# Performance work log

Measured on AMD Instinct MI355X. Metric: run time of the kernel, lower is better.

The kernel has to match this reference:

```python
import jax, jax.numpy as jnp
import numpy as np

T = 0.07        # temperature (hardcoded in CCM)
BN_EPS = 1e-5   # torch BatchNorm1d default eps (eval mode, running stats)


def _l2norm(x):
    # torch F.normalize(dim=1): x / max(||x||, 1e-12)
    n = jnp.linalg.norm(x, axis=1, keepdims=True)
    return x / jnp.maximum(n, 1e-12)


def _attn(q, k):
    # cosine similarity scaled by 1/t and 1/sqrt(num_keys)
    scale = jnp.asarray(k.shape[0], q.dtype) ** 0.5
    return (_l2norm(q) @ _l2norm(k).T) / T / scale


def setup_inputs() -> dict:
    key = jax.random.key(0)
    ks = jax.random.split(key, 24)
    D, N, BS, C, H = 2048, 1024, 64, 65, 128
    f32 = jnp.float32
    def g(k, shape, scale=1.0):
        return jax.random.normal(k, shape, f32) * scale
    return {
        "all_f": g(ks[0], (BS, D)),
        "embedding": _l2norm(g(ks[1], (N, D))),  # memory queue (normalized at init)
        "all_y": jax.random.randint(ks[2], (BS,), 0, C),
        "head_w1": g(ks[3], (D, H), 1.0 / np.sqrt(D)),
        "head_b1": jnp.zeros((H,), f32),
        "head_g": jax.random.uniform(ks[4], (H,), f32) + 0.5,
        "head_beta": g(ks[5], (H,), 0.1),
        "head_rm": g(ks[6], (H,), 0.1),
        "head_rv": jax.random.uniform(ks[7], (H,), f32) + 0.5,
        "head_w2": g(ks[8], (H, H), 1.0 / np.sqrt(H)),
        "head_b2": jnp.zeros((H,), f32),
        "mix_w1": g(ks[9], (2 * H, H), 1.0 / np.sqrt(2 * H)),
        "mix_b1": jnp.zeros((H,), f32),
        "mix_g": jax.random.uniform(ks[10], (H,), f32) + 0.5,
        "mix_beta": g(ks[11], (H,), 0.1),
        "mix_rm": g(ks[12], (H,), 0.1),
        "mix_rv": jax.random.uniform(ks[13], (H,), f32) + 0.5,
        "mix_w2": g(ks[14], (H, D), 1.0 / np.sqrt(H)),
        "mix_b2": jnp.zeros((D,), f32),
        "clf_w": g(ks[15], (D, C), 1.0 / np.sqrt(D)),
        "clf_b": jnp.zeros((C,), f32),
    }


def reference(all_f, embedding, all_y,
              head_w1, head_b1, head_g, head_beta, head_rm, head_rv, head_w2, head_b2,
              mix_w1, mix_b1, mix_g, mix_beta, mix_rm, mix_rv, mix_w2, mix_b2,
              clf_w, clf_b):
    # CCM.causal(all_f, embedding, all_y): returns [bs, num_classes]
    H = head_b2.shape[0]
    # z|x attention over the memory queue
    z_x = jax.nn.softmax(_attn(all_f, embedding), axis=-1)          # [bs, N]

    def head(x):
        h = x @ head_w1 + head_b1
        h = (h - head_rm) * jax.lax.rsqrt(head_rv + BN_EPS) * head_g + head_beta
        return jax.nn.relu(h) @ head_w2 + head_b2                   # [., 128]

    hf = head(all_f)        # [bs, 128]
    hz = head(embedding)    # [N, 128]
    # mixer layer 1 on concat([hf, hz]) decomposed into two matmuls + broadcast add
    h1 = hf @ mix_w1[:H] + mix_b1                                   # [bs, 128]
    h1 = h1[:, None, :] + (hz @ mix_w1[H:])[None, :, :]             # [bs, N, 128]
    h1 = (h1 - mix_rm) * jax.lax.rsqrt(mix_rv + BN_EPS) * mix_g + mix_beta
    h1 = jax.nn.relu(h1)
    mixed = h1 @ mix_w2 + mix_b2                                    # [bs, N, D]
    y_zx = jax.nn.softmax(mixed @ clf_w + clf_b, axis=-1)           # [bs, N, C] = p(y|z,x)
    # p(x): self-attention row-sums, softmax over the batch (all_y given -> this branch)
    p_x = jax.nn.softmax(_attn(all_f, all_f).sum(axis=1), axis=0)   # [bs]
    sum_x = jnp.einsum('b,bnc->nc', p_x, y_zx)                      # [N, C]
    return z_x @ sum_x                                              # [bs, C]
```

## Files before the change

### kernel.cpp

```cpp
#include <hip/hip_runtime.h>
#include <hip/hip_bf16.h>
#include <math.h>

#define D   2048
#define NQ  1024
#define BSZ 64
#define NC  65
#define HD  128

#define OFF_SCALEH 0
#define OFF_CH     128
#define OFF_BZC    256
#define OFF_BAC    384
#define OFF_BVEC   512
#define OFF_PXP    640
#define OFF_WC     896
#define OFF_A2T    6016
#define OFF_B2     14208
#define OFF_SP     145280
#define OFF_SUMX   669568
#define OFF_FNB    751488
#define OFF_AFB    817024
#define OFF_EMBB   882560
#define OFF_W1T    1931136
#define OFF_WZT    2062208
#define OFF_WAT    2070400
#define OFF_MW2B   2078592
#define OFF_CWT    2226048

typedef __attribute__((ext_vector_type(8))) short    bf16x8;
typedef __attribute__((ext_vector_type(4))) float    f32x4;
typedef __attribute__((ext_vector_type(8))) unsigned short u16x8;
typedef __attribute__((ext_vector_type(2))) unsigned short u16x2;

__device__ inline unsigned short f2b(float v) {
    __hip_bfloat16 h = __float2bfloat16(v);
    return __builtin_bit_cast(unsigned short, h);
}

__global__ void __launch_bounds__(256) k_prep(const float* __restrict__ all_f,
                                              const float* __restrict__ emb,
                                              const float* __restrict__ head_w1,
                                              const float* __restrict__ head_b1,
                                              const float* __restrict__ head_g,
                                              const float* __restrict__ head_beta,
                                              const float* __restrict__ head_rm,
                                              const float* __restrict__ head_rv,
                                              const float* __restrict__ head_w2,
                                              const float* __restrict__ head_b2,
                                              const float* __restrict__ mix_w1,
                                              const float* __restrict__ mix_b1,
                                              const float* __restrict__ mix_g,
                                              const float* __restrict__ mix_beta,
                                              const float* __restrict__ mix_rm,
                                              const float* __restrict__ mix_rv,
                                              const float* __restrict__ mix_w2,
                                              const float* __restrict__ mix_b2,
                                              const float* __restrict__ clf_w,
                                              float* __restrict__ ws) {
    __shared__ float sbuf[128*66];
    int bid = blockIdx.x, t = threadIdx.x;
    if (bid == 0) {
        int h = t & 127, jq = t >> 7;
        float sb = 0.f, sa = 0.f;
        #pragma unroll 8
        for (int j = jq*64; j < jq*64 + 64; ++j) {
            float b2v = head_b2[j];
            sb = fmaf(b2v, mix_w1[(HD + j)*HD + h], sb);
            sa = fmaf(b2v, mix_w1[j*HD + h], sa);
        }
        sbuf[jq*256 + h]       = sb;
        sbuf[jq*256 + 128 + h] = sa;
        __syncthreads();
        if (jq == 0) {
            float s = head_g[h] * rsqrtf(head_rv[h] + 1e-5f);
            ws[OFF_SCALEH + h] = s;
            ws[OFF_CH + h] = (head_b1[h] - head_rm[h]) * s + head_beta[h];
            float ms = mix_g[h] * rsqrtf(mix_rv[h] + 1e-5f);
            float msh = mix_beta[h] - mix_rm[h] * ms;
            float sbT = sbuf[h] + sbuf[256 + h];
            float saT = sbuf[128 + h] + sbuf[256 + 128 + h];
            ws[OFF_BZC + h] = sbT * ms;
            ws[OFF_BAC + h] = fmaf(saT + mix_b1[h], ms, msh);
        }
    } else if (bid < 129) {
        int j = bid - 1;
        int h = t & 127, which = t >> 7;
        const float* M1 = mix_w1 + (which ? 0 : HD*HD);
        float ms = mix_g[h] * rsqrtf(mix_rv[h] + 1e-5f);
        float acc = 0.f;
        #pragma unroll 8
        for (int k = 0; k < HD; ++k)
            acc = fmaf(head_w2[j*HD + k], M1[k*HD + h], acc);
        unsigned short* dst = (unsigned short*)(ws + (which ? OFF_WAT : OFF_WZT));
        dst[h*HD + j] = f2b(acc * ms);
    } else if (bid < 147) {
        int r0 = (bid - 129) * 8;
        unsigned short* dst = (unsigned short*)(ws + OFF_MW2B);
        int i0 = t * 8;
        for (int rr = 0; rr < 8; ++rr) {
            int r = r0 + rr;
            u16x8 o;
            if (r < HD || r == HD) {
                const float* src = (r < HD) ? (mix_w2 + (size_t)r * D) : mix_b2;
                float4 f1 = *(const float4*)(src + i0);
                float4 f2 = *(const float4*)(src + i0 + 4);
                o[0]=f2b(f1.x); o[1]=f2b(f1.y); o[2]=f2b(f1.z); o[3]=f2b(f1.w);
                o[4]=f2b(f2.x); o[5]=f2b(f2.y); o[6]=f2b(f2.z); o[7]=f2b(f2.w);
            } else {
                o[0]=0;o[1]=0;o[2]=0;o[3]=0;o[4]=0;o[5]=0;o[6]=0;o[7]=0;
            }
            *(u16x8*)(dst + (size_t)r*D + i0) = o;
        }
    } else if (bid < 163) {
        int k0 = (bid - 147) * 128;
        float (*tile)[66] = (float(*)[66])sbuf;
        for (int i = t; i < 128*65; i += 256) {
            int r = i / 65;
            tile[r][i - 65*r] = clf_w[(size_t)k0*65 + i];
        }
        __syncthreads();
        unsigned short* cwt = (unsigned short*)(ws + OFF_CWT);
        for (int idx = t; idx < 80*16; idx += 256) {
            int c = idx >> 4, kq = idx & 15;
            u16x8 v;
            #pragma unroll
            for (int j = 0; j < 8; ++j)
                v[j] = (c < NC) ? f2b(tile[kq*8 + j][c]) : (unsigned short)0;
            *(u16x8*)(cwt + (size_t)c*D + k0 + kq*8) = v;
        }
    } else if (bid < 227) {
        int b = bid - 163;
        const float* src = all_f + (size_t)b * D;
        int i0 = t * 8;
        float4 f1 = *(const float4*)(src + i0);
        float4 f2 = *(const float4*)(src + i0 + 4);
        float s = f1.x*f1.x + f1.y*f1.y + f1.z*f1.z + f1.w*f1.w
                + f2.x*f2.x + f2.y*f2.y + f2.z*f2.z + f2.w*f2.w;
        sbuf[t] = s; __syncthreads();
        for (int k = 128; k > 0; k >>= 1) { if (t < k) sbuf[t] += sbuf[t + k]; __syncthreads(); }
        float rn = 1.f / fmaxf(sqrtf(sbuf[0]), 1e-12f);
        unsigned short* fnb = (unsigned short*)(ws + OFF_FNB) + (size_t)b * D;
        unsigned short* afb = (unsigned short*)(ws + OFF_AFB) + (size_t)b * D;
        u16x8 on, oa;
        on[0]=f2b(f1.x*rn); on[1]=f2b(f1.y*rn); on[2]=f2b(f1.z*rn); on[3]=f2b(f1.w*rn);
        on[4]=f2b(f2.x*rn); on[5]=f2b(f2.y*rn); on[6]=f2b(f2.z*rn); on[7]=f2b(f2.w*rn);
        oa[0]=f2b(f1.x); oa[1]=f2b(f1.y); oa[2]=f2b(f1.z); oa[3]=f2b(f1.w);
        oa[4]=f2b(f2.x); oa[5]=f2b(f2.y); oa[6]=f2b(f2.z); oa[7]=f2b(f2.w);
        *(u16x8*)(fnb + i0) = on;
        *(u16x8*)(afb + i0) = oa;
    } else if (bid < 483) {
        int n0 = (bid - 227) * 4;
        unsigned short* dst = (unsigned short*)(ws + OFF_EMBB);
        int i0 = t * 8;
        for (int r = 0; r < 4; ++r) {
            const float* src = emb + (size_t)(n0 + r) * D;
            float4 f1 = *(const float4*)(src + i0);
            float4 f2 = *(const float4*)(src + i0 + 4);
            u16x8 o;
            o[0]=f2b(f1.x); o[1]=f2b(f1.y); o[2]=f2b(f1.z); o[3]=f2b(f1.w);
            o[4]=f2b(f2.x); o[5]=f2b(f2.y); o[6]=f2b(f2.z); o[7]=f2b(f2.w);
            *(u16x8*)(dst + (size_t)(n0 + r)*D + i0) = o;
        }
    } else {
        int rb = bid - 483;
        float (*tile)[33] = (float(*)[33])sbuf;
        int k0 = (rb >> 2) * 128, h0 = (rb & 3) * 32;
        int hh = t & 31, kk = t >> 5;
        for (int r = 0; r < 16; ++r)
            tile[kk + r*8][hh] = head_w1[(size_t)(k0 + kk + r*8)*HD + h0 + hh];
        __syncthreads();
        unsigned short* dst = (unsigned short*)(ws + OFF_W1T);
        int kcol = (t & 63) * 2, hrow = t >> 6;
        for (int r = 0; r < 8; ++r) {
            int h = hrow + r*4;
            u16x2 v;
            v[0] = f2b(tile[kcol][h]);
            v[1] = f2b(tile[kcol + 1][h]);
            *(u16x2*)(dst + (size_t)(h0 + h)*D + k0 + kcol) = v;
        }
    }
}

__global__ void __launch_bounds__(512) k_main(const float* __restrict__ clf_b,
                                              float* __restrict__ ws) {
    __shared__ float part[2][32][128];
    __shared__ unsigned short ush[32][136];
    __shared__ float wcp[8][16][16];
    int bid = blockIdx.x, t = threadIdx.x;
    int lane = t & 63, wv = t >> 6;
    int row16 = lane & 15, kgrp = lane >> 4;
    if (bid < 128) {
        const unsigned short* fnb  = (const unsigned short*)(ws + OFF_FNB);
        const unsigned short* embb = (const unsigned short*)(ws + OFF_EMBB);
        int nt = bid & 15, ks = bid >> 4;
        int b0 = (wv & 3) * 16;
        int n0 = nt*64 + (wv >> 2) * 32;
        const unsigned short* Ap = fnb  + (size_t)(b0 + row16)*D + ks*256 + kgrp*8;
        const unsigned short* B0 = embb + (size_t)(n0 + row16)*D + ks*256 + kgrp*8;
        const unsigned short* B1 = B0 + 16*D;
        f32x4 a0 = {0,0,0,0}, a1 = {0,0,0,0};
        #pragma unroll
        for (int s = 0; s < 8; ++s) {
            bf16x8 a = *(const bf16x8*)(Ap + s*32);
            a0 = __builtin_amdgcn_mfma_f32_16x16x32_bf16(a, *(const bf16x8*)(B0 + s*32), a0, 0, 0, 0);
            a1 = __builtin_amdgcn_mfma_f32_16x16x32_bf16(a, *(const bf16x8*)(B1 + s*32), a1, 0, 0, 0);
        }
        float* Sp = ws + OFF_SP + (size_t)ks * BSZ * NQ;
        #pragma unroll
        for (int r = 0; r < 4; ++r) {
            float* rowp = Sp + (size_t)(b0 + kgrp*4 + r)*NQ + n0;
            rowp[row16]      = a0[r];
            rowp[16 + row16] = a1[r];
        }
    } else if (bid < 162) {
        int tile = bid - 128;
        bool isF = tile >= 32;
        const unsigned short* Arow = isF
            ? (const unsigned short*)(ws + OFF_AFB) + (size_t)(tile - 32) * 32 * D
            : (const unsigned short*)(ws + OFF_EMBB) + (size_t)tile * 32 * D;
        const unsigned short* w1t = (const unsigned short*)(ws + OFF_W1T);
        int hgrp = wv & 3, kh = wv >> 2;
        const unsigned short* Ap = Arow + (size_t)row16*D + kh*1024 + kgrp*8;
        const unsigned short* B0 = w1t + (size_t)(hgrp*32 + row16)*D + kh*1024 + kgrp*8;
        const unsigned short* B1 = B0 + 16*D;
        f32x4 h00 = {0,0,0,0}, h01 = {0,0,0,0}, h10 = {0,0,0,0}, h11 = {0,0,0,0};
        #pragma unroll 4
        for (int s = 0; s < 32; ++s) {
            bf16x8 a0 = *(const bf16x8*)(Ap + s*32);
            bf16x8 a1 = *(const bf16x8*)(Ap + 16*D + s*32);
            bf16x8 b0 = *(const bf16x8*)(B0 + s*32);
            bf16x8 b1 = *(const bf16x8*)(B1 + s*32);
            h00 = __builtin_amdgcn_mfma_f32_16x16x32_bf16(a0, b0, h00, 0, 0, 0);
            h01 = __builtin_amdgcn_mfma_f32_16x16x32_bf16(a0, b1, h01, 0, 0, 0);
            h10 = __builtin_amdgcn_mfma_f32_16x16x32_bf16(a1, b0, h10, 0, 0, 0);
            h11 = __builtin_amdgcn_mfma_f32_16x16x32_bf16(a1, b1, h11, 0, 0, 0);
        }
        int mb = kgrp*4, hc0 = hgrp*32 + row16, hc1 = hc0 + 16;
        #pragma unroll
        for (int r = 0; r < 4; ++r) {
            part[kh][mb + r][hc0]      = h00[r];
            part[kh][mb + r][hc1]      = h01[r];
            part[kh][16 + mb + r][hc0] = h10[r];
            part[kh][16 + mb + r][hc1] = h11[r];
        }
        __syncthreads();
        {
            int row = t >> 4, cg = (t & 15) * 8;
            #pragma unroll
            for (int j = 0; j < 8; ++j) {
                int col = cg + j;
                float v = part[0][row][col] + part[1][row][col];
                ush[row][col] = f2b(fmaxf(fmaf(v, ws[OFF_SCALEH + col], ws[OFF_CH + col]), 0.f));
            }
        }
        __syncthreads();
        {
            int rt = wv >> 2, wv2 = wv & 3;
            const unsigned short* wt = (const unsigned short*)(ws + (isF ? OFF_WAT : OFF_WZT));
            const unsigned short* W0 = wt + (size_t)(wv2*32 + row16)*HD + kgrp*8;
            const unsigned short* W1b = W0 + 16*HD;
            f32x4 o0 = {0,0,0,0}, o1 = {0,0,0,0};
            #pragma unroll
            for (int s = 0; s < 4; ++s) {
                bf16x8 a = *(const bf16x8*)(&ush[rt*16 + row16][s*32 + kgrp*8]);
                o0 = __builtin_amdgcn_mfma_f32_16x16x32_bf16(a, *(const bf16x8*)(W0 + s*32), o0, 0, 0, 0);
                o1 = __builtin_amdgcn_mfma_f32_16x16x32_bf16(a, *(const bf16x8*)(W1b + s*32), o1, 0, 0, 0);
            }
            int hcA = wv2*32 + row16, hcB = hcA + 16;
            int boff = isF ? OFF_BAC : OFF_BZC;
            float bz0 = ws[boff + hcA], bz1 = ws[boff + hcB];
            float* outp = isF ? (ws + OFF_A2T + (size_t)(tile - 32)*32*HD)
                              : (ws + OFF_B2  + (size_t)tile*32*HD);
            #pragma unroll
            for (int r = 0; r < 4; ++r) {
                outp[(size_t)(rt*16 + mb + r)*HD + hcA] = o0[r] + bz0;
                outp[(size_t)(rt*16 + mb + r)*HD + hcB] = o1[r] + bz1;
            }
        }
    } else if (bid < 207) {
        int w = bid - 162;
        int mt = w / 5, ntile = w % 5;
        const unsigned short* mw2b = (const unsigned short*)(ws + OFF_MW2B);
        const unsigned short* cwt  = (const unsigned short*)(ws + OFF_CWT);
        const unsigned short* Ap = mw2b + (size_t)(mt*16 + row16)*D + wv*256 + kgrp*8;
        const unsigned short* Bp = cwt  + (size_t)(ntile*16 + row16)*D + wv*256 + kgrp*8;
        f32x4 acc = {0,0,0,0};
        #pragma unroll
        for (int s = 0; s < 8; ++s)
            acc = __builtin_amdgcn_mfma_f32_16x16x32_bf16(
                *(const bf16x8*)(Ap + s*32), *(const bf16x8*)(Bp + s*32), acc, 0, 0, 0);
        #pragma unroll
        for (int r = 0; r < 4; ++r)
            wcp[wv][kgrp*4 + r][row16] = acc[r];
        __syncthreads();
        if (t < 256) {
            int j = t >> 4, c16 = t & 15;
            float s = 0.f;
            #pragma unroll
            for (int q = 0; q < 8; ++q) s += wcp[q][j][c16];
            int jj = mt*16 + j, c = ntile*16 + c16;
            unsigned short* wct = (unsigned short*)(ws + OFF_WC);
            if (jj < HD)       wct[(size_t)c*HD + jj] = f2b(s);
            else if (jj == HD) ws[OFF_BVEC + c] = (c < NC) ? s + clf_b[c] : -1e30f;
        }
    } else {
        int pb = bid - 207;
        const unsigned short* fnb = (const unsigned short*)(ws + OFF_FNB);
        int bq = wv & 3, kq = (wv >> 2) + pb*2;
        int b0 = bq*16;
        const unsigned short* Ap = fnb + (size_t)(b0 + row16)*D + kq*512 + kgrp*8;
        const unsigned short* Bp = fnb + (size_t)row16*D + kq*512 + kgrp*8;
        f32x4 acc[4];
        #pragma unroll
        for (int nt = 0; nt < 4; ++nt) acc[nt] = (f32x4){0.f,0.f,0.f,0.f};
        #pragma unroll 2
        for (int s = 0; s < 16; ++s) {
            bf16x8 a = *(const bf16x8*)(Ap + s*32);
            #pragma unroll
            for (int nt = 0; nt < 4; ++nt)
                acc[nt] = __builtin_amdgcn_mfma_f32_16x16x32_bf16(
                    a, *(const bf16x8*)(Bp + (size_t)nt*16*D + s*32), acc[nt], 0, 0, 0);
        }
        #pragma unroll
        for (int r = 0; r < 4; ++r) {
            float v = acc[0][r] + acc[1][r] + acc[2][r] + acc[3][r];
            v += __shfl_xor(v, 1); v += __shfl_xor(v, 2);
            v += __shfl_xor(v, 4); v += __shfl_xor(v, 8);
            if (row16 == 0)
                ws[OFF_PXP + kq*64 + b0 + kgrp*4 + r] = v;
        }
    }
}

__global__ void __launch_bounds__(256) k_mix_mfma(float* __restrict__ ws) {
    __shared__ unsigned short wcs[80][136];
    __shared__ float redp[4][80];
    int t = threadIdx.x, lane = t & 63, wv = t >> 6;
    int n = blockIdx.x;
    int row16 = lane & 15, kgrp = lane >> 4;
    const unsigned short* wct = (const unsigned short*)(ws + OFF_WC);
    for (int i = t; i < 80*16; i += 256) {
        int r = i >> 4, cc = (i & 15) * 8;
        *(u16x8*)&wcs[r][cc] = *(const u16x8*)(wct + (size_t)r*HD + cc);
    }
    const float invTS = 1.0f / (0.07f * 8.0f);
    float sv = (ws[OFF_PXP + lane] + ws[OFF_PXP + 64 + lane]
              + ws[OFF_PXP + 128 + lane] + ws[OFF_PXP + 192 + lane]) * invTS;
    float m2 = sv;
    m2 = fmaxf(m2, __shfl_xor(m2, 1));  m2 = fmaxf(m2, __shfl_xor(m2, 2));
    m2 = fmaxf(m2, __shfl_xor(m2, 4));  m2 = fmaxf(m2, __shfl_xor(m2, 8));
    m2 = fmaxf(m2, __shfl_xor(m2, 16)); m2 = fmaxf(m2, __shfl_xor(m2, 32));
    float e2 = __expf(sv - m2);
    float su = e2;
    su += __shfl_xor(su, 1);  su += __shfl_xor(su, 2);  su += __shfl_xor(su, 4);
    su += __shfl_xor(su, 8);  su += __shfl_xor(su, 16); su += __shfl_xor(su, 32);
    float px = e2 / su;

    float bvl[5];
    #pragma unroll
    for (int ct = 0; ct < 5; ++ct) bvl[ct] = ws[OFF_BVEC + ct*16 + row16];
    __syncthreads();

    const float* b2r = ws + OFF_B2 + (size_t)n * HD;
    const float* a2r = ws + OFF_A2T + (size_t)(wv*16 + row16) * HD;
    bf16x8 af[4];
    #pragma unroll
    for (int kt = 0; kt < 4; ++kt) {
        const float* ap = a2r + kt*32 + kgrp*8;
        const float* bp = b2r + kt*32 + kgrp*8;
        float4 alo = *(const float4*)(ap);
        float4 ahi = *(const float4*)(ap + 4);
        float4 blo = *(const float4*)(bp);
        float4 bhi = *(const float4*)(bp + 4);
        bf16x8 v;
        v[0] = (short)f2b(fmaxf(alo.x + blo.x, 0.f));
        v[1] = (short)f2b(fmaxf(alo.y + blo.y, 0.f));
        v[2] = (short)f2b(fmaxf(alo.z + blo.z, 0.f));
        v[3] = (short)f2b(fmaxf(alo.w + blo.w, 0.f));
        v[4] = (short)f2b(fmaxf(ahi.x + bhi.x, 0.f));
        v[5] = (short)f2b(fmaxf(ahi.y + bhi.y, 0.f));
        v[6] = (short)f2b(fmaxf(ahi.z + bhi.z, 0.f));
        v[7] = (short)f2b(fmaxf(ahi.w + bhi.w, 0.f));
        af[kt] = v;
    }
    f32x4 acc[5];
    #pragma unroll
    for (int ct = 0; ct < 5; ++ct) acc[ct] = (f32x4){0.f,0.f,0.f,0.f};
    #pragma unroll
    for (int ct = 0; ct < 5; ++ct)
        #pragma unroll
        for (int kt = 0; kt < 4; ++kt)
            acc[ct] = __builtin_amdgcn_mfma_f32_16x16x32_bf16(
                af[kt], *(const bf16x8*)(&wcs[ct*16 + row16][kt*32 + kgrp*8]), acc[ct], 0, 0, 0);

    float outp[5] = {0.f, 0.f, 0.f, 0.f, 0.f};
    #pragma unroll
    for (int r = 0; r < 4; ++r) {
        float v0 = acc[0][r] + bvl[0];
        float v1 = acc[1][r] + bvl[1];
        float v2 = acc[2][r] + bvl[2];
        float v3 = acc[3][r] + bvl[3];
        float v4 = acc[4][r] + bvl[4];
        float m = fmaxf(fmaxf(fmaxf(v0, v1), fmaxf(v2, v3)), v4);
        m = fmaxf(m, __shfl_xor(m, 1)); m = fmaxf(m, __shfl_xor(m, 2));
        m = fmaxf(m, __shfl_xor(m, 4)); m = fmaxf(m, __shfl_xor(m, 8));
        float e0 = __expf(v0 - m), e1 = __expf(v1 - m), e2v = __expf(v2 - m);
        float e3 = __expf(v3 - m), e4 = __expf(v4 - m);
        float s = e0 + e1 + e2v + e3 + e4;
        s += __shfl_xor(s, 1); s += __shfl_xor(s, 2);
        s += __shfl_xor(s, 4); s += __shfl_xor(s, 8);
        float pxr = __shfl(px, wv*16 + kgrp*4 + r);
        float scale = pxr / s;
        outp[0] = fmaf(e0, scale, outp[0]);
        outp[1] = fmaf(e1, scale, outp[1]);
        outp[2] = fmaf(e2v, scale, outp[2]);
        outp[3] = fmaf(e3, scale, outp[3]);
        outp[4] = fmaf(e4, scale, outp[4]);
    }
    #pragma unroll
    for (int ct = 0; ct < 5; ++ct) {
        float v = outp[ct];
        v += __shfl_xor(v, 16); v += __shfl_xor(v, 32);
        outp[ct] = v;
    }
    if (kgrp == 0) {
        #pragma unroll
        for (int ct = 0; ct < 5; ++ct) redp[wv][ct*16 + row16] = outp[ct];
    }
    __syncthreads();
    if (t < 80) {
        ws[OFF_SUMX + (size_t)n*80 + t] = redp[0][t] + redp[1][t] + redp[2][t] + redp[3][t];
    }
}

__global__ void __launch_bounds__(512) k_outz(const float* __restrict__ ws, float* __restrict__ out) {
    __shared__ float red8m[8], red8s[8];
    __shared__ float zrow[NQ];
    __shared__ float parts[8][128];
    int b = blockIdx.x, t = threadIdx.x;
    int lane = t & 63, wvv = t >> 6;
    const float invTS = 1.0f / (0.07f * 32.0f);
    const float* Sp = ws + OFF_SP + (size_t)b * NQ;
    float v0, v1;
    {
        float s = 0.f;
        #pragma unroll
        for (int p = 0; p < 8; ++p) s += Sp[(size_t)p*BSZ*NQ + t];
        v0 = s * invTS;
        s = 0.f;
        #pragma unroll
        for (int p = 0; p < 8; ++p) s += Sp[(size_t)p*BSZ*NQ + 512 + t];
        v1 = s * invTS;
    }
    float vmax = fmaxf(v0, v1);
    vmax = fmaxf(vmax, __shfl_xor(vmax, 1));  vmax = fmaxf(vmax, __shfl_xor(vmax, 2));
    vmax = fmaxf(vmax, __shfl_xor(vmax, 4));  vmax = fmaxf(vmax, __shfl_xor(vmax, 8));
    vmax = fmaxf(vmax, __shfl_xor(vmax, 16)); vmax = fmaxf(vmax, __shfl_xor(vmax, 32));
    if (lane == 0) red8m[wvv] = vmax;
    __syncthreads();
    float m = red8m[0];
    #pragma unroll
    for (int q = 1; q < 8; ++q) m = fmaxf(m, red8m[q]);
    float e0 = __expf(v0 - m), e1 = __expf(v1 - m);
    float ss = e0 + e1;
    ss += __shfl_xor(ss, 1);  ss += __shfl_xor(ss, 2);  ss += __shfl_xor(ss, 4);
    ss += __shfl_xor(ss, 8);  ss += __shfl_xor(ss, 16); ss += __shfl_xor(ss, 32);
    if (lane == 0) red8s[wvv] = ss;
    __syncthreads();
    float S = red8s[0] + red8s[1] + red8s[2] + red8s[3]
            + red8s[4] + red8s[5] + red8s[6] + red8s[7];
    float inv = 1.f / S;
    zrow[t]       = e0 * inv;
    zrow[512 + t] = e1 * inv;
    __syncthreads();
    const float* Sx = ws + OFF_SUMX;
    int c2 = 64 + (lane & 15);
    int nbase = wvv * 128;
    float a0 = 0.f, a1 = 0.f;
    #pragma unroll 8
    for (int k = 0; k < 128; ++k) {
        float z = zrow[nbase + k];
        const float* srow = Sx + (size_t)(nbase + k) * 80;
        a0 = fmaf(z, srow[lane], a0);
        a1 = fmaf(z, srow[c2], a1);
    }
    parts[wvv][lane] = a0;
    if (lane < 16) parts[wvv][64 + lane] = a1;
    __syncthreads();
    if (t < NC) {
        float s = 0.f;
        #pragma unroll
        for (int q = 0; q < 8; ++q) s += parts[q][t];
        out[b*NC + t] = s;
    }
}

extern "C" void kernel_launch(void* const* d_in, const int* in_sizes, int n_in,
                              void* d_out, int out_size, void* d_ws, size_t ws_size,
                              hipStream_t stream) {
    const float* all_f    = (const float*)d_in[0];
    const float* emb      = (const float*)d_in[1];
    const float* head_w1  = (const float*)d_in[3];
    const float* head_b1  = (const float*)d_in[4];
    const float* head_g   = (const float*)d_in[5];
    const float* head_beta= (const float*)d_in[6];
    const float* head_rm  = (const float*)d_in[7];
    const float* head_rv  = (const float*)d_in[8];
    const float* head_w2  = (const float*)d_in[9];
    const float* head_b2  = (const float*)d_in[10];
    const float* mix_w1   = (const float*)d_in[11];
    const float* mix_b1   = (const float*)d_in[12];
    const float* mix_g    = (const float*)d_in[13];
    const float* mix_beta = (const float*)d_in[14];
    const float* mix_rm   = (const float*)d_in[15];
    const float* mix_rv   = (const float*)d_in[16];
    const float* mix_w2   = (const float*)d_in[17];
    const float* mix_b2   = (const float*)d_in[18];
    const float* clf_w    = (const float*)d_in[19];
    const float* clf_b    = (const float*)d_in[20];
    float* ws  = (float*)d_ws;
    float* out = (float*)d_out;

    hipLaunchKernelGGL(k_prep, dim3(547), dim3(256), 0, stream,
                       all_f, emb, head_w1, head_b1, head_g, head_beta, head_rm, head_rv,
                       head_w2, head_b2, mix_w1, mix_b1, mix_g, mix_beta, mix_rm, mix_rv,
                       mix_w2, mix_b2, clf_w, ws);
    hipLaunchKernelGGL(k_main,     dim3(209),  dim3(512), 0, stream, clf_b, ws);
    hipLaunchKernelGGL(k_mix_mfma, dim3(1024), dim3(256), 0, stream, ws);
    hipLaunchKernelGGL(k_outz,     dim3(64),   dim3(512), 0, stream, ws, out);
}
```

Before: 65.67 us.

## Fuse mixer and output kernels with atomic ticket tail, rebalance prep grid

```diff
diff --git a/kernel.cpp b/kernel.cpp
--- a/kernel.cpp
+++ b/kernel.cpp
@@ -13,6 +13,7 @@
 #define OFF_BZC    256
 #define OFF_BAC    384
 #define OFF_BVEC   512
+#define OFF_TICK   600
 #define OFF_PXP    640
 #define OFF_WC     896
 #define OFF_A2T    6016
@@ -94,11 +95,11 @@
             acc = fmaf(head_w2[j*HD + k], M1[k*HD + h], acc);
         unsigned short* dst = (unsigned short*)(ws + (which ? OFF_WAT : OFF_WZT));
         dst[h*HD + j] = f2b(acc * ms);
-    } else if (bid < 147) {
-        int r0 = (bid - 129) * 8;
+    } else if (bid < 165) {
+        int r0 = (bid - 129) * 4;
         unsigned short* dst = (unsigned short*)(ws + OFF_MW2B);
         int i0 = t * 8;
-        for (int rr = 0; rr < 8; ++rr) {
+        for (int rr = 0; rr < 4; ++rr) {
             int r = r0 + rr;
             u16x8 o;
             if (r < HD || r == HD) {
@@ -112,8 +113,8 @@
             }
             *(u16x8*)(dst + (size_t)r*D + i0) = o;
         }
-    } else if (bid < 163) {
-        int k0 = (bid - 147) * 128;
+    } else if (bid < 181) {
+        int k0 = (bid - 165) * 128;
         float (*tile)[66] = (float(*)[66])sbuf;
         for (int i = t; i < 128*65; i += 256) {
             int r = i / 65;
@@ -129,17 +130,20 @@
                 v[j] = (c < NC) ? f2b(tile[kq*8 + j][c]) : (unsigned short)0;
             *(u16x8*)(cwt + (size_t)c*D + k0 + kq*8) = v;
         }
-    } else if (bid < 227) {
-        int b = bid - 163;
+    } else if (bid < 245) {
+        int b = bid - 181;
         const float* src = all_f + (size_t)b * D;
         int i0 = t * 8;
         float4 f1 = *(const float4*)(src + i0);
         float4 f2 = *(const float4*)(src + i0 + 4);
         float s = f1.x*f1.x + f1.y*f1.y + f1.z*f1.z + f1.w*f1.w
                 + f2.x*f2.x + f2.y*f2.y + f2.z*f2.z + f2.w*f2.w;
-        sbuf[t] = s; __syncthreads();
-        for (int k = 128; k > 0; k >>= 1) { if (t < k) sbuf[t] += sbuf[t + k]; __syncthreads(); }
-        float rn = 1.f / fmaxf(sqrtf(sbuf[0]), 1e-12f);
+        s += __shfl_xor(s, 1);  s += __shfl_xor(s, 2);  s += __shfl_xor(s, 4);
+        s += __shfl_xor(s, 8);  s += __shfl_xor(s, 16); s += __shfl_xor(s, 32);
+        if ((t & 63) == 0) sbuf[t >> 6] = s;
+        __syncthreads();
+        float tot = sbuf[0] + sbuf[1] + sbuf[2] + sbuf[3];
+        float rn = 1.f / fmaxf(sqrtf(tot), 1e-12f);
         unsigned short* fnb = (unsigned short*)(ws + OFF_FNB) + (size_t)b * D;
         unsigned short* afb = (unsigned short*)(ws + OFF_AFB) + (size_t)b * D;
         u16x8 on, oa;
@@ -149,11 +153,11 @@
         oa[4]=f2b(f2.x); oa[5]=f2b(f2.y); oa[6]=f2b(f2.z); oa[7]=f2b(f2.w);
         *(u16x8*)(fnb + i0) = on;
         *(u16x8*)(afb + i0) = oa;
-    } else if (bid < 483) {
-        int n0 = (bid - 227) * 4;
+    } else if (bid < 757) {
+        int n0 = (bid - 245) * 2;
         unsigned short* dst = (unsigned short*)(ws + OFF_EMBB);
         int i0 = t * 8;
-        for (int r = 0; r < 4; ++r) {
+        for (int r = 0; r < 2; ++r) {
             const float* src = emb + (size_t)(n0 + r) * D;
             float4 f1 = *(const float4*)(src + i0);
             float4 f2 = *(const float4*)(src + i0 + 4);
@@ -163,7 +167,7 @@
             *(u16x8*)(dst + (size_t)(n0 + r)*D + i0) = o;
         }
     } else {
-        int rb = bid - 483;
+        int rb = bid - 757;
         float (*tile)[33] = (float(*)[33])sbuf;
         int k0 = (rb >> 2) * 128, h0 = (rb & 3) * 32;
         int hh = t & 31, kk = t >> 5;
@@ -183,7 +187,8 @@
 }
 
 __global__ void __launch_bounds__(512) k_main(const float* __restrict__ clf_b,
-                                              float* __restrict__ ws) {
+                                              float* __restrict__ ws,
+                                              float* __restrict__ out) {
     __shared__ float part[2][32][128];
     __shared__ unsigned short ush[32][136];
     __shared__ float wcp[8][16][16];
@@ -272,10 +277,11 @@
             float bz0 = ws[boff + hcA], bz1 = ws[boff + hcB];
             float* outp = isF ? (ws + OFF_A2T + (size_t)(tile - 32)*32*HD)
                               : (ws + OFF_B2  + (size_t)tile*32*HD);
+            int mb2 = kgrp*4;
             #pragma unroll
             for (int r = 0; r < 4; ++r) {
-                outp[(size_t)(rt*16 + mb + r)*HD + hcA] = o0[r] + bz0;
-                outp[(size_t)(rt*16 + mb + r)*HD + hcB] = o1[r] + bz1;
+                outp[(size_t)(rt*16 + mb2 + r)*HD + hcA] = o0[r] + bz0;
+                outp[(size_t)(rt*16 + mb2 + r)*HD + hcB] = o1[r] + bz1;
             }
         }
     } else if (bid < 207) {
@@ -306,6 +312,8 @@
         }
     } else {
         int pb = bid - 207;
+        for (int i = t; i < 2080; i += 512) out[pb*2080 + i] = 0.f;
+        if (pb == 0 && t == 0) *(unsigned*)(ws + OFF_TICK) = 0u;
         const unsigned short* fnb = (const unsigned short*)(ws + OFF_FNB);
         int bq = wv & 3, kq = (wv >> 2) + pb*2;
         int b0 = bq*16;
@@ -333,113 +341,138 @@
     }
 }
 
-__global__ void __launch_bounds__(256) k_mix_mfma(float* __restrict__ ws) {
-    __shared__ unsigned short wcs[80][136];
-    __shared__ float redp[4][80];
-    int t = threadIdx.x, lane = t & 63, wv = t >> 6;
-    int n = blockIdx.x;
+__global__ void __launch_bounds__(512) k_mixz(float* __restrict__ ws, float* __restrict__ out) {
+    union SU {
+        struct { unsigned short wcs[80][136]; float a2s[64][132]; float redp[8][80]; } p2;
+        struct { float red8m[8]; float red8s[8]; float zrow[NQ]; float parts[8][80]; } p3;
+    };
+    __shared__ SU su;
+    __shared__ unsigned tk_s;
+    int bid = blockIdx.x, t = threadIdx.x;
+    int lane = t & 63, wv = t >> 6;
     int row16 = lane & 15, kgrp = lane >> 4;
-    const unsigned short* wct = (const unsigned short*)(ws + OFF_WC);
-    for (int i = t; i < 80*16; i += 256) {
-        int r = i >> 4, cc = (i & 15) * 8;
-        *(u16x8*)&wcs[r][cc] = *(const u16x8*)(wct + (size_t)r*HD + cc);
-    }
-    const float invTS = 1.0f / (0.07f * 8.0f);
-    float sv = (ws[OFF_PXP + lane] + ws[OFF_PXP + 64 + lane]
-              + ws[OFF_PXP + 128 + lane] + ws[OFF_PXP + 192 + lane]) * invTS;
-    float m2 = sv;
-    m2 = fmaxf(m2, __shfl_xor(m2, 1));  m2 = fmaxf(m2, __shfl_xor(m2, 2));
-    m2 = fmaxf(m2, __shfl_xor(m2, 4));  m2 = fmaxf(m2, __shfl_xor(m2, 8));
-    m2 = fmaxf(m2, __shfl_xor(m2, 16)); m2 = fmaxf(m2, __shfl_xor(m2, 32));
-    float e2 = __expf(sv - m2);
-    float su = e2;
-    su += __shfl_xor(su, 1);  su += __shfl_xor(su, 2);  su += __shfl_xor(su, 4);
-    su += __shfl_xor(su, 8);  su += __shfl_xor(su, 16); su += __shfl_xor(su, 32);
-    float px = e2 / su;
-
-    float bvl[5];
-    #pragma unroll
-    for (int ct = 0; ct < 5; ++ct) bvl[ct] = ws[OFF_BVEC + ct*16 + row16];
-    __syncthreads();
-
-    const float* b2r = ws + OFF_B2 + (size_t)n * HD;
-    const float* a2r = ws + OFF_A2T + (size_t)(wv*16 + row16) * HD;
-    bf16x8 af[4];
-    #pragma unroll
-    for (int kt = 0; kt < 4; ++kt) {
-        const float* ap = a2r + kt*32 + kgrp*8;
-        const float* bp = b2r + kt*32 + kgrp*8;
-        float4 alo = *(const float4*)(ap);
-        float4 ahi = *(const float4*)(ap + 4);
-        float4 blo = *(const float4*)(bp);
-        float4 bhi = *(const float4*)(bp + 4);
-        bf16x8 v;
-        v[0] = (short)f2b(fmaxf(alo.x + blo.x, 0.f));
-        v[1] = (short)f2b(fmaxf(alo.y + blo.y, 0.f));
-        v[2] = (short)f2b(fmaxf(alo.z + blo.z, 0.f));
-        v[3] = (short)f2b(fmaxf(alo.w + blo.w, 0.f));
-        v[4] = (short)f2b(fmaxf(ahi.x + bhi.x, 0.f));
-        v[5] = (short)f2b(fmaxf(ahi.y + bhi.y, 0.f));
-        v[6] = (short)f2b(fmaxf(ahi.z + bhi.z, 0.f));
-        v[7] = (short)f2b(fmaxf(ahi.w + bhi.w, 0.f));
-        af[kt] = v;
-    }
-    f32x4 acc[5];
-    #pragma unroll
-    for (int ct = 0; ct < 5; ++ct) acc[ct] = (f32x4){0.f,0.f,0.f,0.f};
-    #pragma unroll
-    for (int ct = 0; ct < 5; ++ct)
-        #pragma unroll
-        for (int kt = 0; kt < 4; ++kt)
-            acc[ct] = __builtin_amdgcn_mfma_f32_16x16x32_bf16(
-                af[kt], *(const bf16x8*)(&wcs[ct*16 + row16][kt*32 + kgrp*8]), acc[ct], 0, 0, 0);
-
-    float outp[5] = {0.f, 0.f, 0.f, 0.f, 0.f};
-    #pragma unroll
-    for (int r = 0; r < 4; ++r) {
-        float v0 = acc[0][r] + bvl[0];
-        float v1 = acc[1][r] + bvl[1];
-        float v2 = acc[2][r] + bvl[2];
-        float v3 = acc[3][r] + bvl[3];
-        float v4 = acc[4][r] + bvl[4];
-        float m = fmaxf(fmaxf(fmaxf(v0, v1), fmaxf(v2, v3)), v4);
-        m = fmaxf(m, __shfl_xor(m, 1)); m = fmaxf(m, __shfl_xor(m, 2));
-        m = fmaxf(m, __shfl_xor(m, 4)); m = fmaxf(m, __shfl_xor(m, 8));
-        float e0 = __expf(v0 - m), e1 = __expf(v1 - m), e2v = __expf(v2 - m);
-        float e3 = __expf(v3 - m), e4 = __expf(v4 - m);
-        float s = e0 + e1 + e2v + e3 + e4;
-        s += __shfl_xor(s, 1); s += __shfl_xor(s, 2);
-        s += __shfl_xor(s, 4); s += __shfl_xor(s, 8);
-        float pxr = __shfl(px, wv*16 + kgrp*4 + r);
-        float scale = pxr / s;
-        outp[0] = fmaf(e0, scale, outp[0]);
-        outp[1] = fmaf(e1, scale, outp[1]);
-        outp[2] = fmaf(e2v, scale, outp[2]);
-        outp[3] = fmaf(e3, scale, outp[3]);
-        outp[4] = fmaf(e4, scale, outp[4]);
-    }
-    #pragma unroll
-    for (int ct = 0; ct < 5; ++ct) {
-        float v = outp[ct];
-        v += __shfl_xor(v, 16); v += __shfl_xor(v, 32);
-        outp[ct] = v;
-    }
-    if (kgrp == 0) {
-        #pragma unroll
-        for (int ct = 0; ct < 5; ++ct) redp[wv][ct*16 + row16] = outp[ct];
-    }
-    __syncthreads();
-    if (t < 80) {
-        ws[OFF_SUMX + (size_t)n*80 + t] = redp[0][t] + redp[1][t] + redp[2][t] + redp[3][t];
-    }
-}
-
-__global__ void __launch_bounds__(512) k_outz(const float* __restrict__ ws, float* __restrict__ out) {
-    __shared__ float red8m[8], red8s[8];
-    __shared__ float zrow[NQ];
-    __shared__ float parts[8][128];
-    int b = blockIdx.x, t = threadIdx.x;
-    int lane = t & 63, wvv = t >> 6;
+
+    {
+        const unsigned short* wct = (const unsigned short*)(ws + OFF_WC);
+        for (int i = t; i < 80*16; i += 512) {
+            int r = i >> 4, cc = (i & 15) * 8;
+            *(u16x8*)&su.p2.wcs[r][cc] = *(const u16x8*)(wct + (size_t)r*HD + cc);
+        }
+        const float* a2g = ws + OFF_A2T;
+        for (int i = t; i < 64*32; i += 512) {
+            int r = i >> 5, q = i & 31;
+            *(float4*)&su.p2.a2s[r][q*4] = *(const float4*)(a2g + (size_t)r*HD + q*4);
+        }
+        const float invTS = 1.0f / (0.07f * 8.0f);
+        float sv = (ws[OFF_PXP + lane] + ws[OFF_PXP + 64 + lane]
+                  + ws[OFF_PXP + 128 + lane] + ws[OFF_PXP + 192 + lane]) * invTS;
+        float m2 = sv;
+        m2 = fmaxf(m2, __shfl_xor(m2, 1));  m2 = fmaxf(m2, __shfl_xor(m2, 2));
+        m2 = fmaxf(m2, __shfl_xor(m2, 4));  m2 = fmaxf(m2, __shfl_xor(m2, 8));
+        m2 = fmaxf(m2, __shfl_xor(m2, 16)); m2 = fmaxf(m2, __shfl_xor(m2, 32));
+        float e2 = __expf(sv - m2);
+        float ssum = e2;
+        ssum += __shfl_xor(ssum, 1);  ssum += __shfl_xor(ssum, 2);  ssum += __shfl_xor(ssum, 4);
+        ssum += __shfl_xor(ssum, 8);  ssum += __shfl_xor(ssum, 16); ssum += __shfl_xor(ssum, 32);
+        float px = e2 / ssum;
+        float bvl[5];
+        #pragma unroll
+        for (int ct = 0; ct < 5; ++ct) bvl[ct] = ws[OFF_BVEC + ct*16 + row16];
+        __syncthreads();
+        int bt = wv & 3, ng = wv >> 2;
+        int n = bid*2 + ng;
+        const float* b2r = ws + OFF_B2 + (size_t)n * HD;
+        bf16x8 af[4];
+        #pragma unroll
+        for (int kt = 0; kt < 4; ++kt) {
+            const float* ap = &su.p2.a2s[bt*16 + row16][kt*32 + kgrp*8];
+            float4 alo = *(const float4*)(ap);
+            float4 ahi = *(const float4*)(ap + 4);
+            float4 blo = *(const float4*)(b2r + kt*32 + kgrp*8);
+            float4 bhi = *(const float4*)(b2r + kt*32 + kgrp*8 + 4);
+            bf16x8 v;
+            v[0] = (short)f2b(fmaxf(alo.x + blo.x, 0.f));
+            v[1] = (short)f2b(fmaxf(alo.y + blo.y, 0.f));
+            v[2] = (short)f2b(fmaxf(alo.z + blo.z, 0.f));
+            v[3] = (short)f2b(fmaxf(alo.w + blo.w, 0.f));
+            v[4] = (short)f2b(fmaxf(ahi.x + bhi.x, 0.f));
+            v[5] = (short)f2b(fmaxf(ahi.y + bhi.y, 0.f));
+            v[6] = (short)f2b(fmaxf(ahi.z + bhi.z, 0.f));
+            v[7] = (short)f2b(fmaxf(ahi.w + bhi.w, 0.f));
+            af[kt] = v;
+        }
+        f32x4 acc[5];
+        #pragma unroll
+        for (int ct = 0; ct < 5; ++ct) acc[ct] = (f32x4){0.f,0.f,0.f,0.f};
+        #pragma unroll
+        for (int ct = 0; ct < 5; ++ct)
+            #pragma unroll
+            for (int kt = 0; kt < 4; ++kt)
+                acc[ct] = __builtin_amdgcn_mfma_f32_16x16x32_bf16(
+                    af[kt], *(const bf16x8*)(&su.p2.wcs[ct*16 + row16][kt*32 + kgrp*8]),
+                    acc[ct], 0, 0, 0);
+        float outp[5] = {0.f, 0.f, 0.f, 0.f, 0.f};
+        #pragma unroll
+        for (int r = 0; r < 4; ++r) {
+            float v0 = acc[0][r] + bvl[0];
+            float v1 = acc[1][r] + bvl[1];
+            float v2 = acc[2][r] + bvl[2];
+            float v3 = acc[3][r] + bvl[3];
+            float v4 = acc[4][r] + bvl[4];
+            float m = fmaxf(fmaxf(fmaxf(v0, v1), fmaxf(v2, v3)), v4);
+            m = fmaxf(m, __shfl_xor(m, 1)); m = fmaxf(m, __shfl_xor(m, 2));
+            m = fmaxf(m, __shfl_xor(m, 4)); m = fmaxf(m, __shfl_xor(m, 8));
+            float e0 = __expf(v0 - m), e1 = __expf(v1 - m), e2v = __expf(v2 - m);
+            float e3 = __expf(v3 - m), e4 = __expf(v4 - m);
+            float s = e0 + e1 + e2v + e3 + e4;
+            s += __shfl_xor(s, 1); s += __shfl_xor(s, 2);
+            s += __shfl_xor(s, 4); s += __shfl_xor(s, 8);
+            float pxr = __shfl(px, bt*16 + kgrp*4 + r);
+            float scale = pxr / s;
+            outp[0] = fmaf(e0, scale, outp[0]);
+            outp[1] = fmaf(e1, scale, outp[1]);
+            outp[2] = fmaf(e2v, scale, outp[2]);
+            outp[3] = fmaf(e3, scale, outp[3]);
+            outp[4] = fmaf(e4, scale, outp[4]);
+        }
+        #pragma unroll
+        for (int ct = 0; ct < 5; ++ct) {
+            float v = outp[ct];
+            v += __shfl_xor(v, 16); v += __shfl_xor(v, 32);
+            outp[ct] = v;
+        }
+        if (kgrp == 0) {
+            #pragma unroll
+            for (int ct = 0; ct < 5; ++ct) su.p2.redp[wv][ct*16 + row16] = outp[ct];
+        }
+        __syncthreads();
+        if (t < 160) {
+            int half = (t >= 80) ? 1 : 0;
+            int c = t - 80*half;
+            int nn = bid*2 + half;
+            float v = su.p2.redp[half*4 + 0][c] + su.p2.redp[half*4 + 1][c]
+                    + su.p2.redp[half*4 + 2][c] + su.p2.redp[half*4 + 3][c];
+            __hip_atomic_store(ws + OFF_SUMX + (size_t)nn*80 + c, v,
+                               __ATOMIC_RELAXED, __HIP_MEMORY_SCOPE_AGENT);
+        }
+    }
+    __syncthreads();
+    if (t == 0)
+        tk_s = __hip_atomic_fetch_add((unsigned*)(ws + OFF_TICK), 1u,
+                                      __ATOMIC_ACQ_REL, __HIP_MEMORY_SCOPE_AGENT);
+    __syncthreads();
+    unsigned old = tk_s;
+    if (old < 384u) return;
+
+    if (t == 0) {
+        while (__hip_atomic_load((unsigned*)(ws + OFF_TICK),
+                                 __ATOMIC_ACQUIRE, __HIP_MEMORY_SCOPE_AGENT) < 512u)
+            __builtin_amdgcn_s_sleep(1);
+    }
+    __syncthreads();
+
+    int idx = (int)old - 384;
+    int b = idx >> 1, half = idx & 1;
     const float invTS = 1.0f / (0.07f * 32.0f);
     const float* Sp = ws + OFF_SP + (size_t)b * NQ;
     float v0, v1;
@@ -457,42 +490,44 @@
     vmax = fmaxf(vmax, __shfl_xor(vmax, 1));  vmax = fmaxf(vmax, __shfl_xor(vmax, 2));
     vmax = fmaxf(vmax, __shfl_xor(vmax, 4));  vmax = fmaxf(vmax, __shfl_xor(vmax, 8));
     vmax = fmaxf(vmax, __shfl_xor(vmax, 16)); vmax = fmaxf(vmax, __shfl_xor(vmax, 32));
-    if (lane == 0) red8m[wvv] = vmax;
-    __syncthreads();
-    float m = red8m[0];
+    if (lane == 0) su.p3.red8m[wv] = vmax;
+    __syncthreads();
+    float m = su.p3.red8m[0];
     #pragma unroll
-    for (int q = 1; q < 8; ++q) m = fmaxf(m, red8m[q]);
+    for (int q = 1; q < 8; ++q) m = fmaxf(m, su.p3.red8m[q]);
     float e0 = __expf(v0 - m), e1 = __expf(v1 - m);
     float ss = e0 + e1;
     ss += __shfl_xor(ss, 1);  ss += __shfl_xor(ss, 2);  ss += __shfl_xor(ss, 4);
     ss += __shfl_xor(ss, 8);  ss += __shfl_xor(ss, 16); ss += __shfl_xor(ss, 32);
-    if (lane == 0) red8s[wvv] = ss;
-    __syncthreads();
-    float S = red8s[0] + red8s[1] + red8s[2] + red8s[3]
-            + red8s[4] + red8s[5] + red8s[6] + red8s[7];
+    if (lane == 0) su.p3.red8s[wv] = ss;
+    __syncthreads();
+    float S = su.p3.red8s[0] + su.p3.red8s[1] + su.p3.red8s[2] + su.p3.red8s[3]
+            + su.p3.red8s[4] + su.p3.red8s[5] + su.p3.red8s[6] + su.p3.red8s[7];
     float inv = 1.f / S;
-    zrow[t]       = e0 * inv;
-    zrow[512 + t] = e1 * inv;
+    su.p3.zrow[t]       = e0 * inv;
+    su.p3.zrow[512 + t] = e1 * inv;
     __syncthreads();
     const float* Sx = ws + OFF_SUMX;
     int c2 = 64 + (lane & 15);
-    int nbase = wvv * 128;
+    int nbase = half*512 + wv*64;
     float a0 = 0.f, a1 = 0.f;
-    #pragma unroll 8
-    for (int k = 0; k < 128; ++k) {
-        float z = zrow[nbase + k];
+    #pragma unroll 4
+    for (int k = 0; k < 64; ++k) {
+        float z = su.p3.zrow[nbase + k];
         const float* srow = Sx + (size_t)(nbase + k) * 80;
-        a0 = fmaf(z, srow[lane], a0);
-        a1 = fmaf(z, srow[c2], a1);
-    }
-    parts[wvv][lane] = a0;
-    if (lane < 16) parts[wvv][64 + lane] = a1;
+        float s0 = __hip_atomic_load(srow + lane, __ATOMIC_RELAXED, __HIP_MEMORY_SCOPE_AGENT);
+        float s1 = __hip_atomic_load(srow + c2,   __ATOMIC_RELAXED, __HIP_MEMORY_SCOPE_AGENT);
+        a0 = fmaf(z, s0, a0);
+        a1 = fmaf(z, s1, a1);
+    }
+    su.p3.parts[wv][lane] = a0;
+    if (lane < 16) su.p3.parts[wv][64 + lane] = a1;
     __syncthreads();
     if (t < NC) {
         float s = 0.f;
         #pragma unroll
-        for (int q = 0; q < 8; ++q) s += parts[q][t];
-        out[b*NC + t] = s;
+        for (int q = 0; q < 8; ++q) s += su.p3.parts[q][t];
+        atomicAdd(&out[b*NC + t], s);
     }
 }
 
@@ -522,11 +557,10 @@
     float* ws  = (float*)d_ws;
     float* out = (float*)d_out;
 
-    hipLaunchKernelGGL(k_prep, dim3(547), dim3(256), 0, stream,
+    hipLaunchKernelGGL(k_prep, dim3(821), dim3(256), 0, stream,
                        all_f, emb, head_w1, head_b1, head_g, head_beta, head_rm, head_rv,
                        head_w2, head_b2, mix_w1, mix_b1, mix_g, mix_beta, mix_rm, mix_rv,
                        mix_w2, mix_b2, clf_w, ws);
-    hipLaunchKernelGGL(k_main,     dim3(209),  dim3(512), 0, stream, clf_b, ws);
-    hipLaunchKernelGGL(k_mix_mfma, dim3(1024), dim3(256), 0, stream, ws);
-    hipLaunchKernelGGL(k_outz,     dim3(64),   dim3(512), 0, stream, ws, out);
+    hipLaunchKernelGGL(k_main, dim3(209), dim3(512), 0, stream, clf_b, ws, out);
+    hipLaunchKernelGGL(k_mixz, dim3(512), dim3(512), 0, stream, ws, out);
 }
```

Result: slower. 74.36 us (+13.2%).
